# Kernel optimization log

Hardware: AMD Instinct MI355X
Metric: run time of the kernel (lower is better)

Reference implementation:

```python
import jax, jax.numpy as jnp
import numpy as np

# Config constants (from CantorFusionConfigV2 defaults / init_kwargs)
NUM_HEADS = 8
HEAD_DIM = 64
K_NEIGHBORS = 64        # fusion_window
LEVELS = 5              # k_simplex + 1
TAU = 0.25
BASE = 3.0
ALPHA = 0.5
EPS = 1e-8
RESIDUAL_SCALE = 1.0


def _cantor_measure(S):
    """Vectorized Devil's Staircase Cantor measure for S positions in [0,1]. Returns [S]."""
    pos = (jnp.arange(S, dtype=jnp.float32) + 0.5) / S
    pos = jnp.clip(pos, 1e-10, 1.0 - 1e-10)
    ks = jnp.arange(1, LEVELS + 1, dtype=jnp.float32)
    scales = BASE ** ks                      # [L]
    lvl_w = 0.5 ** ks                        # [L]
    centers = jnp.array([0.5, 1.5, 2.5], dtype=jnp.float32)
    y = jnp.mod(pos[:, None] * scales, BASE)            # [S, L]
    logits = -((y[..., None] - centers) ** 2) / (TAU + 1e-10)  # [S, L, 3]
    p = jax.nn.softmax(logits, axis=-1)
    bits = p[..., 2] + ALPHA * p[..., 1]                # [S, L]
    return jnp.sum(bits * lvl_w, axis=-1)               # [S]


def _routes_and_weights(S):
    """KNN routes [S,K] by Cantor distance + inverse-distance softmax weights [S,K]."""
    cm = _cantor_measure(S)
    Dm = jnp.abs(cm[:, None] - cm[None, :])             # [S, S]
    Dm = Dm / (Dm.max() + 1e-10)
    neg_d, routes = jax.lax.top_k(-Dm, K_NEIGHBORS)     # k smallest distances
    route_dist = -neg_d                                  # [S, K]
    w = jax.nn.softmax(1.0 / (route_dist + EPS), axis=-1)
    return routes, w


def setup_inputs() -> dict:
    key = jax.random.key(0)
    k1, k2, k3 = jax.random.split(key, 3)
    B, S, D = 2, 2048, 512
    x = jax.random.normal(k1, (B, S, D), dtype=jnp.float32)
    W_in = jax.random.normal(k2, (D, D), dtype=jnp.float32) * (1.0 / np.sqrt(D))
    b_in = jnp.zeros((D,), dtype=jnp.float32)
    W_out = jax.random.normal(k3, (D, D), dtype=jnp.float32) * (1.0 / np.sqrt(D))
    b_out = jnp.zeros((D,), dtype=jnp.float32)
    return {"x": x, "W_in": W_in, "b_in": b_in, "W_out": W_out, "b_out": b_out}


def reference(x, W_in, b_in, W_out, b_out):
    B, S, dim = x.shape
    routes, w = _routes_and_weights(S)                   # [S,K], [S,K] (no-grad geometry)
    routes = jax.lax.stop_gradient(routes)
    w = jax.lax.stop_gradient(w)
    # input projection and head split -> [B, H, S, D]
    h = (x @ W_in + b_in).reshape(B, S, NUM_HEADS, HEAD_DIM).transpose(0, 2, 1, 3)
    # neighbor gather [B, H, S, K, D] then inverse-distance weighted sum
    gathered = h[:, :, routes, :]                        # [B,H,S,K,D]
    fused = jnp.einsum('bhskd,sk->bhsd', gathered, w)    # [B,H,S,D]
    out = fused.transpose(0, 2, 1, 3).reshape(B, S, dim) @ W_out + b_out
    return x + RESIDUAL_SCALE * out
```

## Files before the change

### kernel.cpp

```cpp
#include <hip/hip_runtime.h>
#include <hip/hip_bf16.h>

#define S_LEN 2048

typedef __attribute__((ext_vector_type(8))) short bf16x8;
typedef __attribute__((ext_vector_type(4))) float f32x4;
typedef __attribute__((ext_vector_type(4))) unsigned int u32x4;

__device__ inline unsigned short f2b(float f) {
    unsigned u = __builtin_bit_cast(unsigned, f);
    return (unsigned short)((u + 0x7FFFu + ((u >> 16) & 1u)) >> 16);
}

__device__ inline int swoff(int row, int k) {
    int o = row * 128 + k * 2;
    return o ^ ((row & 7) << 4);
}

__global__ __launch_bounds__(256) void cantor_kernel(float* __restrict__ cmf) {
    int s = blockIdx.x * 256 + threadIdx.x;
    float pos = ((float)s + 0.5f) * (1.0f / 2048.0f);
    float cm = 0.0f, scale = 1.0f, lvlw = 1.0f;
    #pragma unroll
    for (int k = 1; k <= 5; ++k) {
        scale *= 3.0f; lvlw *= 0.5f;
        float y = fmodf(pos * scale, 3.0f);
        float d0 = y - 0.5f, d1 = y - 1.5f, d2 = y - 2.5f;
        float l0 = -(d0 * d0) * 4.0f;
        float l1 = -(d1 * d1) * 4.0f;
        float l2 = -(d2 * d2) * 4.0f;
        float m = fmaxf(l0, fmaxf(l1, l2));
        float e0 = (float)exp((double)(l0 - m));
        float e1 = (float)exp((double)(l1 - m));
        float e2 = (float)exp((double)(l2 - m));
        float sum = (e0 + e1) + e2;
        float p1 = e1 / sum, p2 = e2 / sum;
        cm += (p2 + 0.5f * p1) * lvlw;
    }
    cmf[s] = cm;
}

__global__ __launch_bounds__(256) void prep3_kernel(
    const float* __restrict__ x,
    const float* __restrict__ W_in, const float* __restrict__ b_in,
    const float* __restrict__ W_out, const float* __restrict__ b_out,
    const float* __restrict__ cmf,
    unsigned short* __restrict__ Wct, float* __restrict__ bc,
    unsigned short* __restrict__ xa) {
    __shared__ char lds[24576];
    const int b = blockIdx.x, tid = threadIdx.x;
    const int wid = tid >> 6, lane = tid & 63;
    const int l15 = lane & 15, l4 = lane >> 4;

    if (b < 64) {
        char* As = lds;
        char* Bs = lds + 8192;
        int bm = b >> 3, bn = b & 7;
        int wr = wid >> 1, wc = wid & 1;
        int an = tid & 63, ajg = tid >> 6;
        int bk = tid >> 2, bjq = (tid & 3) * 16;
        const float* acol = W_out + bm * 64 + an;
        const float* brow = W_in + (size_t)(bn * 64 + bk) * 512 + bjq;
        f32x4 acc[2][2] = {};
        for (int k0 = 0; k0 < 512; k0 += 64) {
            unsigned short ta[16];
            #pragma unroll
            for (int i = 0; i < 16; ++i)
                ta[i] = f2b(acol[(size_t)(k0 + ajg * 16 + i) * 512]);
            *(u32x4*)(As + swoff(an, ajg * 16))     = *(u32x4*)&ta[0];
            *(u32x4*)(As + swoff(an, ajg * 16 + 8)) = *(u32x4*)&ta[8];
            unsigned short tb[16];
            #pragma unroll
            for (int i = 0; i < 4; ++i) {
                float4 v = *(const float4*)(brow + k0 + i * 4);
                tb[i*4+0] = f2b(v.x); tb[i*4+1] = f2b(v.y);
                tb[i*4+2] = f2b(v.z); tb[i*4+3] = f2b(v.w);
            }
            *(u32x4*)(Bs + swoff(bk, bjq))     = *(u32x4*)&tb[0];
            *(u32x4*)(Bs + swoff(bk, bjq + 8)) = *(u32x4*)&tb[8];
            __syncthreads();
            #pragma unroll
            for (int kk = 0; kk < 2; ++kk) {
                const int kb = kk * 32 + l4 * 8;
                bf16x8 af[2], bg[2];
                #pragma unroll
                for (int m = 0; m < 2; ++m)
                    af[m] = *(bf16x8*)(As + swoff(wr * 32 + m * 16 + l15, kb));
                #pragma unroll
                for (int n = 0; n < 2; ++n)
                    bg[n] = *(bf16x8*)(Bs + swoff(wc * 32 + n * 16 + l15, kb));
                #pragma unroll
                for (int m = 0; m < 2; ++m)
                    #pragma unroll
                    for (int n = 0; n < 2; ++n)
                        acc[m][n] = __builtin_amdgcn_mfma_f32_16x16x32_bf16(
                            af[m], bg[n], acc[m][n], 0, 0, 0);
            }
            __syncthreads();
        }
        #pragma unroll
        for (int m = 0; m < 2; ++m)
            #pragma unroll
            for (int r = 0; r < 4; ++r) {
                int row = bm * 64 + wr * 32 + m * 16 + l4 * 4 + r;
                #pragma unroll
                for (int n = 0; n < 2; ++n) {
                    int col = bn * 64 + wc * 32 + n * 16 + l15;
                    Wct[(size_t)row * 512 + col] = f2b(acc[m][n][r]);
                }
            }
    } else if (b < 72) {
        float (*red)[64] = (float(*)[64])lds;
        int nl = tid & 63, jc = tid >> 6;
        int n = (b - 64) * 64 + nl;
        float acc = 0.0f;
        #pragma unroll 8
        for (int j = jc * 128; j < jc * 128 + 128; ++j)
            acc += b_in[j] * W_out[(size_t)j * 512 + n];
        red[jc][nl] = acc;
        __syncthreads();
        if (jc == 0)
            bc[n] = b_out[n] + ((red[0][nl] + red[1][nl]) +
                                (red[2][nl] + red[3][nl]));
    } else {
        float* cml = (float*)lds;
        int*   mem = (int*)(lds + 8192) + wid * 64;
        for (int i = tid; i < 512; i += 256)
            *(float4*)&cml[i * 4] = *(const float4*)&cmf[i * 4];
        __syncthreads();
        int s = (b - 72) * 4 + wid;
        float v = cml[s];
        int n = 0;
        for (int j0 = 0; j0 < S_LEN; j0 += 64) {
            float c = cml[j0 + lane];
            bool m = (c == v);
            unsigned long long mask = __ballot(m);
            if (m) {
                int idx = n + __popcll(mask & ((1ull << lane) - 1ull));
                if (idx < 64) mem[idx] = j0 + lane;
            }
            n += __popcll(mask);
        }
        int gn = n < 64 ? n : 64;
        float a0[8] = {}, a1[8] = {};
        for (int e = 0; e < gn; ++e) {
            int r = mem[e];
            const float* p0 = x + (size_t)r * 512 + lane * 8;
            const float* p1 = p0 + (size_t)S_LEN * 512;
            float4 u0 = *(const float4*)p0, u1 = *(const float4*)(p0 + 4);
            float4 w0 = *(const float4*)p1, w1 = *(const float4*)(p1 + 4);
            a0[0] += u0.x; a0[1] += u0.y; a0[2] += u0.z; a0[3] += u0.w;
            a0[4] += u1.x; a0[5] += u1.y; a0[6] += u1.z; a0[7] += u1.w;
            a1[0] += w0.x; a1[1] += w0.y; a1[2] += w0.z; a1[3] += w0.w;
            a1[4] += w1.x; a1[5] += w1.y; a1[6] += w1.z; a1[7] += w1.w;
        }
        float gi = 1.0f / (float)gn;
        unsigned short t0[8], t1[8];
        #pragma unroll
        for (int i = 0; i < 8; ++i) {
            t0[i] = f2b(a0[i] * gi);
            t1[i] = f2b(a1[i] * gi);
        }
        *(u32x4*)(xa + (size_t)s * 512 + lane * 8)           = *(u32x4*)t0;
        *(u32x4*)(xa + (size_t)(S_LEN + s) * 512 + lane * 8) = *(u32x4*)t1;
    }
}

__global__ __launch_bounds__(256, 4) void gemmF_kernel(
    const float* __restrict__ x, const unsigned short* __restrict__ xa,
    const unsigned short* __restrict__ Wct, const float* __restrict__ bc,
    float* __restrict__ out) {
    __shared__ char lds[12288];
    char* As = lds;
    char* Bs = lds + 4096;
    const int tid = threadIdx.x;
    const int id = blockIdx.x;
    const int xcd = id & 7, slot = id >> 3;
    const int bm = xcd * 16 + (slot & 15);
    const int bn = slot >> 4;
    const int wid = tid >> 6, lane = tid & 63;
    const int wr = wid >> 1, wc = wid & 1;
    const int l15 = lane & 15, l4 = lane >> 4;
    const int arow = tid >> 3, akq = (tid & 7) * 8;
    const int brow = tid >> 2, bkq = (tid & 3) * 16;

    const unsigned short* asrc = xa  + (size_t)(bm * 32 + arow) * 512 + akq;
    const unsigned short* bsrc = Wct + (size_t)(bn * 64 + brow) * 512 + bkq;

    u32x4 arg, brg[2];
    auto la = [&](int k0) { arg = *(const u32x4*)(asrc + k0); };
    auto lb = [&](int k0) {
        brg[0] = *(const u32x4*)(bsrc + k0);
        brg[1] = *(const u32x4*)(bsrc + k0 + 8);
    };
    auto st = [&]() {
        *(u32x4*)(As + swoff(arow, akq))     = arg;
        *(u32x4*)(Bs + swoff(brow, bkq))     = brg[0];
        *(u32x4*)(Bs + swoff(brow, bkq + 8)) = brg[1];
    };

    f32x4 acc[2] = {};
    la(0); lb(0);
    for (int t = 0; t < 8; ++t) {
        st();
        __syncthreads();
        if (t < 7) { la((t + 1) * 64); lb((t + 1) * 64); }
        #pragma unroll
        for (int kk = 0; kk < 2; ++kk) {
            const int kb = kk * 32 + l4 * 8;
            bf16x8 af = *(bf16x8*)(As + swoff(wr * 16 + l15, kb));
            bf16x8 bg[2];
            #pragma unroll
            for (int n = 0; n < 2; ++n)
                bg[n] = *(bf16x8*)(Bs + swoff(wc * 32 + n * 16 + l15, kb));
            #pragma unroll
            for (int n = 0; n < 2; ++n)
                acc[n] = __builtin_amdgcn_mfma_f32_16x16x32_bf16(
                    af, bg[n], acc[n], 0, 0, 0);
        }
        __syncthreads();
    }

    float bv[2];
    #pragma unroll
    for (int n = 0; n < 2; ++n) bv[n] = bc[bn * 64 + wc * 32 + n * 16 + l15];
    #pragma unroll
    for (int r = 0; r < 4; ++r) {
        int row = bm * 32 + wr * 16 + l4 * 4 + r;
        #pragma unroll
        for (int n = 0; n < 2; ++n) {
            int col = bn * 64 + wc * 32 + n * 16 + l15;
            float v = acc[n][r] + bv[n];
            out[(size_t)row * 512 + col] = x[(size_t)row * 512 + col] + v;
        }
    }
}

extern "C" void kernel_launch(void* const* d_in, const int* in_sizes, int n_in,
                              void* d_out, int out_size, void* d_ws, size_t ws_size,
                              hipStream_t stream) {
    const float* x     = (const float*)d_in[0];
    const float* W_in  = (const float*)d_in[1];
    const float* b_in  = (const float*)d_in[2];
    const float* W_out = (const float*)d_in[3];
    const float* b_out = (const float*)d_in[4];
    float* out = (float*)d_out;

    char* ws = (char*)d_ws;
    unsigned short* Wct = (unsigned short*)ws;
    float*          bc  = (float*)(ws + 524288);
    float*          cmf = (float*)(ws + 524288 + 4096);
    unsigned short* xa  = (unsigned short*)(ws + 524288 + 4096 + 8192);

    cantor_kernel<<<8, 256, 0, stream>>>(cmf);
    prep3_kernel<<<584, 256, 0, stream>>>(x, W_in, b_in, W_out, b_out,
                                          cmf, Wct, bc, xa);
    gemmF_kernel<<<1024, 256, 0, stream>>>(x, xa, Wct, bc, out);
}
```

Measured before the change: 30.16 us.

## Fuse neighbor-average gather into the GEMM and merge cantor into the prep kernel

Drops the separate cantor kernel by running its work in the first blocks of the weight-prep kernel, going from three launches to two. The duplicate-measure row averaging now runs inside the output GEMM: each block builds its 32 averaged bf16 rows in LDS, so the intermediate xa buffer is no longer written to and read back from global memory. The GEMM tile widens to 32x128 with 512 blocks and uses much more LDS, which lowers occupancy. The averaging is also repeated by each of the four column blocks that share a row tile.

Result: slower. 36.37 us (+20.6%).

```diff
diff --git a/kernel.cpp b/kernel.cpp
--- a/kernel.cpp
+++ b/kernel.cpp
@@ -16,46 +16,46 @@
     int o = row * 128 + k * 2;
     return o ^ ((row & 7) << 4);
 }
-
-__global__ __launch_bounds__(256) void cantor_kernel(float* __restrict__ cmf) {
-    int s = blockIdx.x * 256 + threadIdx.x;
-    float pos = ((float)s + 0.5f) * (1.0f / 2048.0f);
-    float cm = 0.0f, scale = 1.0f, lvlw = 1.0f;
-    #pragma unroll
-    for (int k = 1; k <= 5; ++k) {
-        scale *= 3.0f; lvlw *= 0.5f;
-        float y = fmodf(pos * scale, 3.0f);
-        float d0 = y - 0.5f, d1 = y - 1.5f, d2 = y - 2.5f;
-        float l0 = -(d0 * d0) * 4.0f;
-        float l1 = -(d1 * d1) * 4.0f;
-        float l2 = -(d2 * d2) * 4.0f;
-        float m = fmaxf(l0, fmaxf(l1, l2));
-        float e0 = (float)exp((double)(l0 - m));
-        float e1 = (float)exp((double)(l1 - m));
-        float e2 = (float)exp((double)(l2 - m));
-        float sum = (e0 + e1) + e2;
-        float p1 = e1 / sum, p2 = e2 / sum;
-        cm += (p2 + 0.5f * p1) * lvlw;
-    }
-    cmf[s] = cm;
-}
-
-__global__ __launch_bounds__(256) void prep3_kernel(
-    const float* __restrict__ x,
+__device__ inline int xswoff(int row, int k) {
+    int o = row * 1024 + k * 2;
+    return o ^ ((row & 7) << 4);
+}
+
+__global__ __launch_bounds__(256) void prepA_kernel(
     const float* __restrict__ W_in, const float* __restrict__ b_in,
     const float* __restrict__ W_out, const float* __restrict__ b_out,
-    const float* __restrict__ cmf,
-    unsigned short* __restrict__ Wct, float* __restrict__ bc,
-    unsigned short* __restrict__ xa) {
-    __shared__ char lds[24576];
+    float* __restrict__ cmf, unsigned short* __restrict__ Wct,
+    float* __restrict__ bc) {
+    __shared__ char lds[16384];
     const int b = blockIdx.x, tid = threadIdx.x;
     const int wid = tid >> 6, lane = tid & 63;
     const int l15 = lane & 15, l4 = lane >> 4;
 
-    if (b < 64) {
+    if (b < 8) {
+        int s = b * 256 + tid;
+        float pos = ((float)s + 0.5f) * (1.0f / 2048.0f);
+        float cm = 0.0f, scale = 1.0f, lvlw = 1.0f;
+        #pragma unroll
+        for (int k = 1; k <= 5; ++k) {
+            scale *= 3.0f; lvlw *= 0.5f;
+            float y = fmodf(pos * scale, 3.0f);
+            float d0 = y - 0.5f, d1 = y - 1.5f, d2 = y - 2.5f;
+            float l0 = -(d0 * d0) * 4.0f;
+            float l1 = -(d1 * d1) * 4.0f;
+            float l2 = -(d2 * d2) * 4.0f;
+            float m = fmaxf(l0, fmaxf(l1, l2));
+            float e0 = (float)exp((double)(l0 - m));
+            float e1 = (float)exp((double)(l1 - m));
+            float e2 = (float)exp((double)(l2 - m));
+            float sum = (e0 + e1) + e2;
+            float p1 = e1 / sum, p2 = e2 / sum;
+            cm += (p2 + 0.5f * p1) * lvlw;
+        }
+        cmf[s] = cm;
+    } else if (b < 72) {
         char* As = lds;
         char* Bs = lds + 8192;
-        int bm = b >> 3, bn = b & 7;
+        int bb = b - 8, bm = bb >> 3, bn = bb & 7;
         int wr = wid >> 1, wc = wid & 1;
         int an = tid & 63, ajg = tid >> 6;
         int bk = tid >> 2, bjq = (tid & 3) * 16;
@@ -109,10 +109,10 @@
                     Wct[(size_t)row * 512 + col] = f2b(acc[m][n][r]);
                 }
             }
-    } else if (b < 72) {
+    } else {
         float (*red)[64] = (float(*)[64])lds;
         int nl = tid & 63, jc = tid >> 6;
-        int n = (b - 64) * 64 + nl;
+        int n = (b - 72) * 64 + nl;
         float acc = 0.0f;
         #pragma unroll 8
         for (int j = jc * 128; j < jc * 128 + 128; ++j)
@@ -122,116 +122,121 @@
         if (jc == 0)
             bc[n] = b_out[n] + ((red[0][nl] + red[1][nl]) +
                                 (red[2][nl] + red[3][nl]));
-    } else {
-        float* cml = (float*)lds;
-        int*   mem = (int*)(lds + 8192) + wid * 64;
-        for (int i = tid; i < 512; i += 256)
-            *(float4*)&cml[i * 4] = *(const float4*)&cmf[i * 4];
-        __syncthreads();
-        int s = (b - 72) * 4 + wid;
-        float v = cml[s];
-        int n = 0;
-        for (int j0 = 0; j0 < S_LEN; j0 += 64) {
-            float c = cml[j0 + lane];
-            bool m = (c == v);
-            unsigned long long mask = __ballot(m);
-            if (m) {
-                int idx = n + __popcll(mask & ((1ull << lane) - 1ull));
-                if (idx < 64) mem[idx] = j0 + lane;
-            }
-            n += __popcll(mask);
-        }
-        int gn = n < 64 ? n : 64;
-        float a0[8] = {}, a1[8] = {};
-        for (int e = 0; e < gn; ++e) {
-            int r = mem[e];
-            const float* p0 = x + (size_t)r * 512 + lane * 8;
-            const float* p1 = p0 + (size_t)S_LEN * 512;
-            float4 u0 = *(const float4*)p0, u1 = *(const float4*)(p0 + 4);
-            float4 w0 = *(const float4*)p1, w1 = *(const float4*)(p1 + 4);
-            a0[0] += u0.x; a0[1] += u0.y; a0[2] += u0.z; a0[3] += u0.w;
-            a0[4] += u1.x; a0[5] += u1.y; a0[6] += u1.z; a0[7] += u1.w;
-            a1[0] += w0.x; a1[1] += w0.y; a1[2] += w0.z; a1[3] += w0.w;
-            a1[4] += w1.x; a1[5] += w1.y; a1[6] += w1.z; a1[7] += w1.w;
-        }
-        float gi = 1.0f / (float)gn;
-        unsigned short t0[8], t1[8];
-        #pragma unroll
-        for (int i = 0; i < 8; ++i) {
-            t0[i] = f2b(a0[i] * gi);
-            t1[i] = f2b(a1[i] * gi);
-        }
-        *(u32x4*)(xa + (size_t)s * 512 + lane * 8)           = *(u32x4*)t0;
-        *(u32x4*)(xa + (size_t)(S_LEN + s) * 512 + lane * 8) = *(u32x4*)t1;
     }
 }
 
-__global__ __launch_bounds__(256, 4) void gemmF_kernel(
-    const float* __restrict__ x, const unsigned short* __restrict__ xa,
+__global__ __launch_bounds__(256, 3) void gemmG_kernel(
+    const float* __restrict__ x, const float* __restrict__ cmf,
     const unsigned short* __restrict__ Wct, const float* __restrict__ bc,
     float* __restrict__ out) {
-    __shared__ char lds[12288];
-    char* As = lds;
-    char* Bs = lds + 4096;
+    __shared__ char lds[50176];
+    char* xr  = lds;
+    char* BsC = lds + 32768;
     const int tid = threadIdx.x;
+    const int wid = tid >> 6, lane = tid & 63;
+    const int l15 = lane & 15, l4 = lane >> 4;
+    int* mem = (int*)(lds + 49152) + wid * 64;
+
     const int id = blockIdx.x;
     const int xcd = id & 7, slot = id >> 3;
     const int bm = xcd * 16 + (slot & 15);
     const int bn = slot >> 4;
-    const int wid = tid >> 6, lane = tid & 63;
-    const int wr = wid >> 1, wc = wid & 1;
-    const int l15 = lane & 15, l4 = lane >> 4;
-    const int arow = tid >> 3, akq = (tid & 7) * 8;
-    const int brow = tid >> 2, bkq = (tid & 3) * 16;
-
-    const unsigned short* asrc = xa  + (size_t)(bm * 32 + arow) * 512 + akq;
-    const unsigned short* bsrc = Wct + (size_t)(bn * 64 + brow) * 512 + bkq;
-
-    u32x4 arg, brg[2];
-    auto la = [&](int k0) { arg = *(const u32x4*)(asrc + k0); };
-    auto lb = [&](int k0) {
-        brg[0] = *(const u32x4*)(bsrc + k0);
-        brg[1] = *(const u32x4*)(bsrc + k0 + 8);
-    };
-    auto st = [&]() {
-        *(u32x4*)(As + swoff(arow, akq))     = arg;
-        *(u32x4*)(Bs + swoff(brow, bkq))     = brg[0];
-        *(u32x4*)(Bs + swoff(brow, bkq + 8)) = brg[1];
-    };
-
-    f32x4 acc[2] = {};
-    la(0); lb(0);
-    for (int t = 0; t < 8; ++t) {
-        st();
+    const int batch = bm >> 6;
+    const int srow0 = (bm & 63) * 32;
+
+    {
+        float* cml = (float*)BsC;
+        for (int i = tid; i < 512; i += 256)
+            *(float4*)&cml[i * 4] = *(const float4*)&cmf[i * 4];
         __syncthreads();
-        if (t < 7) { la((t + 1) * 64); lb((t + 1) * 64); }
-        #pragma unroll
-        for (int kk = 0; kk < 2; ++kk) {
-            const int kb = kk * 32 + l4 * 8;
-            bf16x8 af = *(bf16x8*)(As + swoff(wr * 16 + l15, kb));
-            bf16x8 bg[2];
-            #pragma unroll
-            for (int n = 0; n < 2; ++n)
-                bg[n] = *(bf16x8*)(Bs + swoff(wc * 32 + n * 16 + l15, kb));
-            #pragma unroll
-            for (int n = 0; n < 2; ++n)
-                acc[n] = __builtin_amdgcn_mfma_f32_16x16x32_bf16(
-                    af, bg[n], acc[n], 0, 0, 0);
-        }
-        __syncthreads();
+        const float* xb = x + (size_t)batch * S_LEN * 512;
+        for (int q = 0; q < 8; ++q) {
+            int sl = wid * 8 + q;
+            int s = srow0 + sl;
+            float v = cml[s];
+            int n = 0;
+            for (int j0 = 0; j0 < S_LEN; j0 += 64) {
+                float c = cml[j0 + lane];
+                bool m = (c == v);
+                unsigned long long mask = __ballot(m);
+                if (m) {
+                    int idx = n + __popcll(mask & ((1ull << lane) - 1ull));
+                    if (idx < 64) mem[idx] = j0 + lane;
+                }
+                n += __popcll(mask);
+            }
+            int gn = n < 64 ? n : 64;
+            float a0[8] = {};
+            for (int e = 0; e < gn; ++e) {
+                const float* p0 = xb + (size_t)mem[e] * 512 + lane * 8;
+                float4 u0 = *(const float4*)p0, u1 = *(const float4*)(p0 + 4);
+                a0[0] += u0.x; a0[1] += u0.y; a0[2] += u0.z; a0[3] += u0.w;
+                a0[4] += u1.x; a0[5] += u1.y; a0[6] += u1.z; a0[7] += u1.w;
+            }
+            float gi = 1.0f / (float)gn;
+            unsigned short t0[8];
+            #pragma unroll
+            for (int i = 0; i < 8; ++i) t0[i] = f2b(a0[i] * gi);
+            *(u32x4*)(xr + xswoff(sl, lane * 8)) = *(u32x4*)t0;
+        }
     }
-
-    float bv[2];
-    #pragma unroll
-    for (int n = 0; n < 2; ++n) bv[n] = bc[bn * 64 + wc * 32 + n * 16 + l15];
-    #pragma unroll
-    for (int r = 0; r < 4; ++r) {
-        int row = bm * 32 + wr * 16 + l4 * 4 + r;
-        #pragma unroll
-        for (int n = 0; n < 2; ++n) {
-            int col = bn * 64 + wc * 32 + n * 16 + l15;
-            float v = acc[n][r] + bv[n];
-            out[(size_t)row * 512 + col] = x[(size_t)row * 512 + col] + v;
+    __syncthreads();
+
+    {
+        char* Bs = BsC;
+        const int wr = wid >> 1, wc = wid & 1;
+        const int brow = tid >> 1, bkh = (tid & 1) * 32;
+        const unsigned short* bsrc =
+            Wct + (size_t)(bn * 128 + brow) * 512 + bkh;
+
+        u32x4 brg[4];
+        auto lb = [&](int k0) {
+            #pragma unroll
+            for (int i = 0; i < 4; ++i)
+                brg[i] = *(const u32x4*)(bsrc + k0 + i * 8);
+        };
+        auto stB = [&]() {
+            #pragma unroll
+            for (int i = 0; i < 4; ++i)
+                *(u32x4*)(Bs + swoff(brow, bkh + i * 8)) = brg[i];
+        };
+
+        f32x4 acc[4] = {};
+        lb(0);
+        for (int t = 0; t < 8; ++t) {
+            stB();
+            __syncthreads();
+            if (t < 7) lb((t + 1) * 64);
+            const int k0 = t * 64;
+            #pragma unroll
+            for (int kk = 0; kk < 2; ++kk) {
+                const int kb = kk * 32 + l4 * 8;
+                bf16x8 af = *(bf16x8*)(xr + xswoff(wr * 16 + l15, k0 + kb));
+                bf16x8 bg[4];
+                #pragma unroll
+                for (int n = 0; n < 4; ++n)
+                    bg[n] = *(bf16x8*)(Bs + swoff(wc * 64 + n * 16 + l15, kb));
+                #pragma unroll
+                for (int n = 0; n < 4; ++n)
+                    acc[n] = __builtin_amdgcn_mfma_f32_16x16x32_bf16(
+                        af, bg[n], acc[n], 0, 0, 0);
+            }
+            __syncthreads();
+        }
+
+        float bv[4];
+        #pragma unroll
+        for (int n = 0; n < 4; ++n)
+            bv[n] = bc[bn * 128 + wc * 64 + n * 16 + l15];
+        #pragma unroll
+        for (int r = 0; r < 4; ++r) {
+            int row = bm * 32 + wr * 16 + l4 * 4 + r;
+            #pragma unroll
+            for (int n = 0; n < 4; ++n) {
+                int col = bn * 128 + wc * 64 + n * 16 + l15;
+                float v = acc[n][r] + bv[n];
+                out[(size_t)row * 512 + col] = x[(size_t)row * 512 + col] + v;
+            }
         }
     }
 }
@@ -250,10 +255,8 @@
     unsigned short* Wct = (unsigned short*)ws;
     float*          bc  = (float*)(ws + 524288);
     float*          cmf = (float*)(ws + 524288 + 4096);
-    unsigned short* xa  = (unsigned short*)(ws + 524288 + 4096 + 8192);
-
-    cantor_kernel<<<8, 256, 0, stream>>>(cmf);
-    prep3_kernel<<<584, 256, 0, stream>>>(x, W_in, b_in, W_out, b_out,
-                                          cmf, Wct, bc, xa);
-    gemmF_kernel<<<1024, 256, 0, stream>>>(x, xa, Wct, bc, out);
-}
+
+    prepA_kernel<<<80, 256, 0, stream>>>(W_in, b_in, W_out, b_out,
+                                         cmf, Wct, bc);
+    gemmG_kernel<<<512, 256, 0, stream>>>(x, cmf, Wct, bc, out);
+}
```
